# Performance work log

Measured on AMD Instinct MI355X. Metric: run time of the kernel, lower is better.

The kernel has to match this reference:

```python
import jax, jax.numpy as jnp
import numpy as np

B, M, S = 4, 1024, 1024
D, H, FF = 1024, 16, 4096
NE, P = 128, 1
HD = D // H
EPS = 1e-5


def _layer_norm(x, g, b):
    mu = x.mean(-1, keepdims=True)
    var = ((x - mu) ** 2).mean(-1, keepdims=True)
    return (x - mu) * jax.lax.rsqrt(var + EPS) * g + b


def _mha(q_in, kv_in, in_w, in_b, out_w, out_b):
    # torch nn.MultiheadAttention: packed in_proj_weight [3D, D], y = x @ W.T + b
    wq, wk, wv = in_w[:D], in_w[D:2 * D], in_w[2 * D:]
    bq, bk, bv = in_b[:D], in_b[D:2 * D], in_b[2 * D:]
    q = (q_in @ wq.T + bq).reshape(q_in.shape[0], q_in.shape[1], H, HD)
    k = (kv_in @ wk.T + bk).reshape(kv_in.shape[0], kv_in.shape[1], H, HD)
    v = (kv_in @ wv.T + bv).reshape(kv_in.shape[0], kv_in.shape[1], H, HD)
    scores = jnp.einsum('bqhd,bkhd->bhqk', q, k) / jnp.sqrt(jnp.float32(HD))
    attn = jax.nn.softmax(scores, axis=-1)
    o = jnp.einsum('bhqk,bkhd->bqhd', attn, v).reshape(q_in.shape[0], q_in.shape[1], D)
    return o @ out_w.T + out_b


def _soft_moe(h, phi, exp_w, exp_b):
    # h: [b, m, FF]; phi: [FF, n, p]
    logits = jnp.einsum('bmd,dnp->bmnp', h, phi)
    dispatch = jax.nn.softmax(logits, axis=1)  # over tokens m
    b, m, n, p = logits.shape
    combine = jax.nn.softmax(logits.reshape(b, m, n * p), axis=-1).reshape(b, m, n, p)
    slots = jnp.einsum('bmd,bmnp->bnpd', h, dispatch)  # [b, n, p, FF]
    y = jnp.einsum('bnpd,ndo->bnpo', slots, exp_w) + exp_b[None, :, None, :]  # [b, n, p, D]
    return jnp.einsum('bnpo,bmnp->bmo', y, combine)


def setup_inputs() -> dict:
    key = jax.random.key(0)
    ks = jax.random.split(key, 16)
    sc = 0.02

    def rn(k, shape):
        return jax.random.normal(k, shape, jnp.float32) * sc

    return {
        'tgt': jax.random.normal(ks[0], (B, M, D), jnp.float32),
        'memory': jax.random.normal(ks[1], (B, S, D), jnp.float32),
        'sa_in_w': rn(ks[2], (3 * D, D)), 'sa_in_b': jnp.zeros((3 * D,), jnp.float32),
        'sa_out_w': rn(ks[3], (D, D)), 'sa_out_b': jnp.zeros((D,), jnp.float32),
        'ca_in_w': rn(ks[4], (3 * D, D)), 'ca_in_b': jnp.zeros((3 * D,), jnp.float32),
        'ca_out_w': rn(ks[5], (D, D)), 'ca_out_b': jnp.zeros((D,), jnp.float32),
        'norm1_g': jnp.ones((D,), jnp.float32), 'norm1_b': jnp.zeros((D,), jnp.float32),
        'norm2_g': jnp.ones((D,), jnp.float32), 'norm2_b': jnp.zeros((D,), jnp.float32),
        'norm3_g': jnp.ones((D,), jnp.float32), 'norm3_b': jnp.zeros((D,), jnp.float32),
        'lin_w': rn(ks[6], (FF, D)), 'lin_b': jnp.zeros((FF,), jnp.float32),
        'phi': rn(ks[7], (FF, NE, P)),
        'exp_w': rn(ks[8], (NE, FF, D)), 'exp_b': jnp.zeros((NE, D), jnp.float32),
    }


def reference(tgt, memory, sa_in_w, sa_in_b, sa_out_w, sa_out_b,
              ca_in_w, ca_in_b, ca_out_w, ca_out_b,
              norm1_g, norm1_b, norm2_g, norm2_b, norm3_g, norm3_b,
              lin_w, lin_b, phi, exp_w, exp_b):
    # post-norm (norm_first=False), dropout=0 (eval)
    x = tgt
    x = _layer_norm(x + _mha(x, x, sa_in_w, sa_in_b, sa_out_w, sa_out_b), norm1_g, norm1_b)
    x = _layer_norm(x + _mha(x, memory, ca_in_w, ca_in_b, ca_out_w, ca_out_b), norm2_g, norm2_b)
    h = jax.nn.relu(x @ lin_w.T + lin_b)  # [B, M, FF]
    ff = _soft_moe(h, phi, exp_w, exp_b)  # [B, M, D]
    x = _layer_norm(x + ff, norm3_g, norm3_b)
    return x
```

## Files before the change

kernel.cpp:

```cpp
#include <hip/hip_runtime.h>
#include <cstdint>
#include <cstddef>

typedef unsigned short u16;
typedef unsigned int   u32;
typedef short bf16x8 __attribute__((ext_vector_type(8)));
typedef float f32x4  __attribute__((ext_vector_type(4)));
typedef u16   u16x8  __attribute__((ext_vector_type(8)));
typedef u16   u16x4  __attribute__((ext_vector_type(4)));
typedef u16   u16x2  __attribute__((ext_vector_type(2)));

constexpr int B_  = 4;
constexpr int M_  = 1024;
constexpr int S_  = 1024;
constexpr int D_  = 1024;
constexpr int H_  = 16;
constexpr int FF_ = 4096;
constexpr int NE_ = 128;

__device__ __forceinline__ u16 f2bf(float f) {
    u32 u = __builtin_bit_cast(u32, f);
    u = (u + 0x7fffu + ((u >> 16) & 1u)) >> 16;
    return (u16)u;
}
__device__ __forceinline__ float bf2f(u16 u) {
    u32 x = ((u32)u) << 16;
    return __builtin_bit_cast(float, x);
}
__device__ __forceinline__ void gload_lds16(const u16* g, u16* l) {
    __builtin_amdgcn_global_load_lds(
        (const __attribute__((address_space(1))) u32*)g,
        (__attribute__((address_space(3))) u32*)l, 16, 0, 0);
}

template<int OUT_BF16, int RELU, int HAS_BIAS>
__global__ __launch_bounds__(256) void gemm_bt_mfma(
    const u16* __restrict__ A, const u16* __restrict__ W,
    const float* __restrict__ bias, void* __restrict__ Cout,
    int K, int N, int lda, int ldw,
    size_t sA, size_t sW, size_t sC)
{
    __shared__ u16 As[128 * 32];
    __shared__ u16 Bs[128 * 32];
    const int tid = threadIdx.x;
    const int w = tid >> 6, l = tid & 63;
    const int bm = blockIdx.y * 128, bn = blockIdx.x * 128;
    const u16* Ab = A + (size_t)blockIdx.z * sA;
    const u16* Wb = W + (size_t)blockIdx.z * sW;

    const int wr = w >> 1, wc = w & 1;
    const int sr = l >> 2;
    const int sk = (l & 3) * 8;
    const u16* aG0 = Ab + (size_t)(bm + w * 16 + sr) * lda + sk;
    const u16* aG1 = Ab + (size_t)(bm + (w + 4) * 16 + sr) * lda + sk;
    const u16* bG0 = Wb + (size_t)(bn + w * 16 + sr) * ldw + sk;
    const u16* bG1 = Wb + (size_t)(bn + (w + 4) * 16 + sr) * ldw + sk;
    u16* aL0 = &As[w * 512];
    u16* aL1 = &As[(w + 4) * 512];
    u16* bL0 = &Bs[w * 512];
    u16* bL1 = &Bs[(w + 4) * 512];

    const int fr = l & 15;
    const int fk = (l >> 4) * 8;

    f32x4 acc[4][4];
#pragma unroll
    for (int i = 0; i < 4; ++i)
#pragma unroll
        for (int j = 0; j < 4; ++j)
#pragma unroll
            for (int q = 0; q < 4; ++q) acc[i][j][q] = 0.f;

    for (int k0 = 0; k0 < K; k0 += 32) {
        __syncthreads();
        gload_lds16(aG0, aL0);
        gload_lds16(aG1, aL1);
        gload_lds16(bG0, bL0);
        gload_lds16(bG1, bL1);
        aG0 += 32; aG1 += 32; bG0 += 32; bG1 += 32;
        __syncthreads();
        bf16x8 af[4], bfr[4];
#pragma unroll
        for (int m = 0; m < 4; ++m)
            af[m] = *(const bf16x8*)&As[(wr * 64 + m * 16 + fr) * 32 + fk];
#pragma unroll
        for (int n = 0; n < 4; ++n)
            bfr[n] = *(const bf16x8*)&Bs[(wc * 64 + n * 16 + fr) * 32 + fk];
#pragma unroll
        for (int m = 0; m < 4; ++m)
#pragma unroll
            for (int n = 0; n < 4; ++n)
                acc[m][n] = __builtin_amdgcn_mfma_f32_16x16x32_bf16(
                    af[m], bfr[n], acc[m][n], 0, 0, 0);
    }

    const int row0 = bm + wr * 64 + (l >> 4) * 4;
    const int col0 = bn + wc * 64;
#pragma unroll
    for (int n = 0; n < 4; ++n) {
        const int col = col0 + n * 16 + fr;
        float bv = 0.f;
        if (HAS_BIAS) bv = bias[col];
#pragma unroll
        for (int m = 0; m < 4; ++m) {
            const int row = row0 + m * 16;
#pragma unroll
            for (int j = 0; j < 4; ++j) {
                float v = acc[m][n][j] + bv;
                if (RELU) v = fmaxf(v, 0.f);
                const size_t idx = (size_t)blockIdx.z * sC + (size_t)(row + j) * N + col;
                if (OUT_BF16) ((u16*)Cout)[idx] = f2bf(v);
                else          ((float*)Cout)[idx] = v;
            }
        }
    }
}

__global__ __launch_bounds__(256) void flash_attn_kernel(
    const u16* __restrict__ Q, int qs,
    const u16* __restrict__ K, int ks,
    const u16* __restrict__ V, int vs,
    u16* __restrict__ O, int Slen)
{
    __shared__ u16 Qs[64][72];
    __shared__ u16 Ks[64][72];
    __shared__ u16 Vt[64][72];
    __shared__ u16 Pw[4][16][72];
    const int b = blockIdx.z, hh = blockIdx.y;
    const int m0 = blockIdx.x * 64;
    const int tid = threadIdx.x;
    const int w = tid >> 6, l = tid & 63;
    const int lq = l & 15, g = l >> 4;

    {
        const int row = tid >> 2, cg = (tid & 3) * 16;
        const u16* qp = Q + ((size_t)b * M_ + m0 + row) * qs + hh * 64 + cg;
        u16x8 v0 = *(const u16x8*)qp;
        u16x8 v1 = *(const u16x8*)(qp + 8);
        u16x8 o0, o1;
#pragma unroll
        for (int i = 0; i < 8; ++i) {
            o0[i] = f2bf(bf2f(v0[i]) * 0.125f);
            o1[i] = f2bf(bf2f(v1[i]) * 0.125f);
        }
        *(u16x8*)&Qs[row][cg]     = o0;
        *(u16x8*)&Qs[row][cg + 8] = o1;
    }
    __syncthreads();
    bf16x8 qf[2];
    qf[0] = *(const bf16x8*)&Qs[w * 16 + lq][g * 8];
    qf[1] = *(const bf16x8*)&Qs[w * 16 + lq][32 + g * 8];

    f32x4 acc_o[4];
#pragma unroll
    for (int nb = 0; nb < 4; ++nb)
#pragma unroll
        for (int j = 0; j < 4; ++j) acc_o[nb][j] = 0.f;
    float m_run = -1e30f, l_run = 0.f;

    const int kp = tid & 31, dg = tid >> 5;
    const int krow = tid >> 2, kcg = (tid & 3) * 16;

    for (int s0 = 0; s0 < Slen; s0 += 64) {
        __syncthreads();
        {
            const u16* kpp = K + ((size_t)b * Slen + s0 + krow) * ks + hh * 64 + kcg;
            *(u16x8*)&Ks[krow][kcg]     = *(const u16x8*)kpp;
            *(u16x8*)&Ks[krow][kcg + 8] = *(const u16x8*)(kpp + 8);
        }
        {
            const u16* vp0 = V + ((size_t)b * Slen + s0 + 2 * kp) * vs + hh * 64 + dg * 8;
            const u16* vp1 = vp0 + vs;
            u16x8 a = *(const u16x8*)vp0;
            u16x8 c = *(const u16x8*)vp1;
#pragma unroll
            for (int i = 0; i < 8; ++i) {
                u16x2 pk; pk[0] = a[i]; pk[1] = c[i];
                *(u16x2*)&Vt[dg * 8 + i][2 * kp] = pk;
            }
        }
        __syncthreads();

        f32x4 s4[4];
#pragma unroll
        for (int mb = 0; mb < 4; ++mb) {
            f32x4 z = {0.f, 0.f, 0.f, 0.f};
            bf16x8 a0 = *(const bf16x8*)&Ks[mb * 16 + lq][g * 8];
            bf16x8 a1 = *(const bf16x8*)&Ks[mb * 16 + lq][32 + g * 8];
            z = __builtin_amdgcn_mfma_f32_16x16x32_bf16(a0, qf[0], z, 0, 0, 0);
            z = __builtin_amdgcn_mfma_f32_16x16x32_bf16(a1, qf[1], z, 0, 0, 0);
            s4[mb] = z;
        }

        float pm = -1e30f;
#pragma unroll
        for (int mb = 0; mb < 4; ++mb)
#pragma unroll
            for (int j = 0; j < 4; ++j) pm = fmaxf(pm, s4[mb][j]);
        pm = fmaxf(pm, __shfl_xor(pm, 16));
        pm = fmaxf(pm, __shfl_xor(pm, 32));

        u16 pbf[4][4];
        float ls = 0.f;
        if (__all(pm - m_run <= 8.f)) {
#pragma unroll
            for (int mb = 0; mb < 4; ++mb)
#pragma unroll
                for (int j = 0; j < 4; ++j) {
                    float p = __expf(s4[mb][j] - m_run);
                    ls += p;
                    pbf[mb][j] = f2bf(p);
                }
            ls += __shfl_xor(ls, 16);
            ls += __shfl_xor(ls, 32);
            l_run += ls;
        } else {
            const float m_new = fmaxf(m_run, pm);
            const float alpha = __expf(m_run - m_new);
#pragma unroll
            for (int mb = 0; mb < 4; ++mb)
#pragma unroll
                for (int j = 0; j < 4; ++j) {
                    float p = __expf(s4[mb][j] - m_new);
                    ls += p;
                    pbf[mb][j] = f2bf(p);
                }
            ls += __shfl_xor(ls, 16);
            ls += __shfl_xor(ls, 32);
            l_run = l_run * alpha + ls;
            m_run = m_new;
            float al[4];
#pragma unroll
            for (int j = 0; j < 4; ++j) al[j] = __shfl(alpha, 4 * g + j);
#pragma unroll
            for (int nb = 0; nb < 4; ++nb)
#pragma unroll
                for (int j = 0; j < 4; ++j) acc_o[nb][j] *= al[j];
        }

#pragma unroll
        for (int mb = 0; mb < 4; ++mb) {
            u16x4 pk;
            pk[0] = pbf[mb][0]; pk[1] = pbf[mb][1];
            pk[2] = pbf[mb][2]; pk[3] = pbf[mb][3];
            *(u16x4*)&Pw[w][lq][mb * 16 + g * 4] = pk;
        }

#pragma unroll
        for (int kc = 0; kc < 2; ++kc) {
            bf16x8 pa = *(const bf16x8*)&Pw[w][lq][kc * 32 + g * 8];
#pragma unroll
            for (int nb = 0; nb < 4; ++nb) {
                bf16x8 bv = *(const bf16x8*)&Vt[nb * 16 + lq][kc * 32 + g * 8];
                acc_o[nb] = __builtin_amdgcn_mfma_f32_16x16x32_bf16(pa, bv, acc_o[nb], 0, 0, 0);
            }
        }
    }

    float linv[4];
#pragma unroll
    for (int j = 0; j < 4; ++j) linv[j] = 1.f / __shfl(l_run, 4 * g + j);
#pragma unroll
    for (int nb = 0; nb < 4; ++nb)
#pragma unroll
        for (int j = 0; j < 4; ++j) {
            const size_t row = (size_t)b * M_ + m0 + w * 16 + 4 * g + j;
            O[row * D_ + hh * 64 + nb * 16 + lq] = f2bf(acc_o[nb][j] * linv[j]);
        }
}

__global__ __launch_bounds__(256) void cvt_multi_kernel(
    const float* __restrict__ s0, u16* __restrict__ d0,
    const float* __restrict__ s1, u16* __restrict__ d1,
    const float* __restrict__ s2, u16* __restrict__ d2,
    const float* __restrict__ s3, u16* __restrict__ d3,
    const float* __restrict__ s4, u16* __restrict__ d4,
    const float* __restrict__ s5, u16* __restrict__ d5,
    const float* __restrict__ s6, u16* __restrict__ d6)
{
    int blk = blockIdx.x;
    const float* s; u16* d;
    if      (blk < 2048) { s = s0; d = d0; }
    else if (blk < 4096) { s = s1; d = d1; blk -= 2048; }
    else if (blk < 5632) { s = s2; d = d2; blk -= 4096; }
    else if (blk < 6144) { s = s3; d = d3; blk -= 5632; }
    else if (blk < 7680) { s = s4; d = d4; blk -= 6144; }
    else if (blk < 8192) { s = s5; d = d5; blk -= 7680; }
    else                 { s = s6; d = d6; blk -= 8192; }
    const size_t i = ((size_t)blk * 256 + threadIdx.x) * 8;
    float4 a = *(const float4*)(s + i);
    float4 b = *(const float4*)(s + i + 4);
    u16x8 o;
    o[0] = f2bf(a.x); o[1] = f2bf(a.y); o[2] = f2bf(a.z); o[3] = f2bf(a.w);
    o[4] = f2bf(b.x); o[5] = f2bf(b.y); o[6] = f2bf(b.z); o[7] = f2bf(b.w);
    *(u16x8*)(d + i) = o;
}

__global__ __launch_bounds__(256) void transpose_f32_bf16_kernel(
    const float* __restrict__ src, u16* __restrict__ dst, int R, int C,
    size_t sI, size_t sO)
{
    __shared__ u16 t[32][33];
    src += (size_t)blockIdx.z * sI;
    dst += (size_t)blockIdx.z * sO;
    const int c0 = blockIdx.x * 32, r0 = blockIdx.y * 32;
    const int x = threadIdx.x & 31, y = threadIdx.x >> 5;
    for (int i = y; i < 32; i += 8)
        t[i][x] = f2bf(src[(size_t)(r0 + i) * C + c0 + x]);
    __syncthreads();
    for (int i = y; i < 32; i += 8)
        dst[(size_t)(c0 + i) * R + r0 + x] = t[x][i];
}

__global__ __launch_bounds__(256) void transpose_bf16_kernel(
    const u16* __restrict__ src, u16* __restrict__ dst, int R, int C,
    size_t sI, size_t sO)
{
    __shared__ u16 t[32][33];
    src += (size_t)blockIdx.z * sI;
    dst += (size_t)blockIdx.z * sO;
    const int c0 = blockIdx.x * 32, r0 = blockIdx.y * 32;
    const int x = threadIdx.x & 31, y = threadIdx.x >> 5;
    for (int i = y; i < 32; i += 8)
        t[i][x] = src[(size_t)(r0 + i) * C + c0 + x];
    __syncthreads();
    for (int i = y; i < 32; i += 8)
        dst[(size_t)(c0 + i) * R + r0 + x] = t[x][i];
}

__global__ __launch_bounds__(256) void resid_ln_kernel(
    const float* __restrict__ X, const float* __restrict__ R,
    const float* __restrict__ g, const float* __restrict__ bt,
    float* __restrict__ Y, u16* __restrict__ Ybf)
{
    __shared__ float s1[4], s2[4];
    const size_t row = blockIdx.x;
    const int tid = threadIdx.x;
    const float4 x4 = *(const float4*)(X + row * 1024 + tid * 4);
    const float4 r4 = *(const float4*)(R + row * 1024 + tid * 4);
    float v[4] = {x4.x + r4.x, x4.y + r4.y, x4.z + r4.z, x4.w + r4.w};
    float s = v[0] + v[1] + v[2] + v[3];
    float q = v[0] * v[0] + v[1] * v[1] + v[2] * v[2] + v[3] * v[3];
#pragma unroll
    for (int off = 32; off; off >>= 1) {
        s += __shfl_xor(s, off);
        q += __shfl_xor(q, off);
    }
    if ((tid & 63) == 0) { s1[tid >> 6] = s; s2[tid >> 6] = q; }
    __syncthreads();
    s = s1[0] + s1[1] + s1[2] + s1[3];
    q = s2[0] + s2[1] + s2[2] + s2[3];
    const float mu = s * (1.f / 1024.f);
    const float var = q * (1.f / 1024.f) - mu * mu;
    const float rinv = rsqrtf(var + 1e-5f);
    const float4 g4 = *(const float4*)(g + tid * 4);
    const float4 b4 = *(const float4*)(bt + tid * 4);
    float o[4];
    o[0] = (v[0] - mu) * rinv * g4.x + b4.x;
    o[1] = (v[1] - mu) * rinv * g4.y + b4.y;
    o[2] = (v[2] - mu) * rinv * g4.z + b4.z;
    o[3] = (v[3] - mu) * rinv * g4.w + b4.w;
    *(float4*)(Y + row * 1024 + tid * 4) = *(float4*)o;
    if (Ybf) {
        u16x4 ob;
        ob[0] = f2bf(o[0]); ob[1] = f2bf(o[1]);
        ob[2] = f2bf(o[2]); ob[3] = f2bf(o[3]);
        *(u16x4*)(Ybf + row * 1024 + tid * 4) = ob;
    }
}

__global__ __launch_bounds__(256) void dispatch_softmax_T_kernel(
    const float* __restrict__ logitsP, u16* __restrict__ dispT)
{
    __shared__ float red[4];
    constexpr size_t CH = (size_t)B_ * M_ * NE_;
    const int n = blockIdx.x, b = blockIdx.y;
    u16* O = dispT + ((size_t)b * NE_ + n) * M_;
    const int tid = threadIdx.x;
    float v[4];
#pragma unroll
    for (int i = 0; i < 4; ++i) {
        const size_t idx = (size_t)(b * M_ + tid + 256 * i) * NE_ + n;
        v[i] = logitsP[idx] + logitsP[CH + idx] + logitsP[2 * CH + idx] + logitsP[3 * CH + idx];
    }
    float mx = fmaxf(fmaxf(v[0], v[1]), fmaxf(v[2], v[3]));
#pragma unroll
    for (int off = 32; off; off >>= 1) mx = fmaxf(mx, __shfl_xor(mx, off));
    if ((tid & 63) == 0) red[tid >> 6] = mx;
    __syncthreads();
    mx = fmaxf(fmaxf(red[0], red[1]), fmaxf(red[2], red[3]));
    __syncthreads();
    float e[4], s = 0.f;
#pragma unroll
    for (int i = 0; i < 4; ++i) { e[i] = __expf(v[i] - mx); s += e[i]; }
#pragma unroll
    for (int off = 32; off; off >>= 1) s += __shfl_xor(s, off);
    if ((tid & 63) == 0) red[tid >> 6] = s;
    __syncthreads();
    s = red[0] + red[1] + red[2] + red[3];
    const float inv = 1.f / s;
#pragma unroll
    for (int i = 0; i < 4; ++i) O[tid + 256 * i] = f2bf(e[i] * inv);
}

__global__ __launch_bounds__(64) void combine_softmax_kernel(
    const float* __restrict__ logitsP, u16* __restrict__ comb)
{
    constexpr size_t CH = (size_t)B_ * M_ * NE_;
    const size_t row = blockIdx.x;
    const int lane = threadIdx.x;
    const size_t i0 = row * NE_ + lane;
    const size_t i1 = i0 + 64;
    float a = logitsP[i0] + logitsP[CH + i0] + logitsP[2 * CH + i0] + logitsP[3 * CH + i0];
    float c = logitsP[i1] + logitsP[CH + i1] + logitsP[2 * CH + i1] + logitsP[3 * CH + i1];
    float mx = fmaxf(a, c);
#pragma unroll
    for (int off = 32; off; off >>= 1) mx = fmaxf(mx, __shfl_xor(mx, off));
    float e0 = __expf(a - mx), e1 = __expf(c - mx);
    float s = e0 + e1;
#pragma unroll
    for (int off = 32; off; off >>= 1) s += __shfl_xor(s, off);
    const float inv = 1.f / s;
    comb[row * NE_ + lane]      = f2bf(e0 * inv);
    comb[row * NE_ + lane + 64] = f2bf(e1 * inv);
}

__global__ __launch_bounds__(256) void expert_partial_kernel(
    const float* __restrict__ slots, const float* __restrict__ exp_w,
    float* __restrict__ part)
{
    __shared__ float sl[4][512];
    const int n = blockIdx.x;
    const int c = blockIdx.y;
    const int f0 = c * 512;
    const int t = threadIdx.x;
    for (int i = t; i < 2048; i += 256) {
        const int b = i >> 9, f = i & 511;
        sl[b][f] = slots[((size_t)b * NE_ + n) * FF_ + f0 + f];
    }
    __syncthreads();
    const int d4 = t * 4;
    const float* wp = exp_w + ((size_t)n * FF_ + f0) * D_ + d4;
    f32x4 acc[4];
#pragma unroll
    for (int b = 0; b < 4; ++b)
#pragma unroll
        for (int j = 0; j < 4; ++j) acc[b][j] = 0.f;
#pragma unroll 4
    for (int f = 0; f < 512; ++f) {
        const float4 w4 = *(const float4*)wp;
        wp += D_;
#pragma unroll
        for (int b = 0; b < 4; ++b) {
            const float s = sl[b][f];
            acc[b][0] = fmaf(s, w4.x, acc[b][0]);
            acc[b][1] = fmaf(s, w4.y, acc[b][1]);
            acc[b][2] = fmaf(s, w4.z, acc[b][2]);
            acc[b][3] = fmaf(s, w4.w, acc[b][3]);
        }
    }
#pragma unroll
    for (int b = 0; b < 4; ++b)
        *(f32x4*)&part[(((size_t)c * 4 + b) * NE_ + n) * D_ + d4] = acc[b];
}

__global__ __launch_bounds__(256) void reduce_yT_kernel(
    const float* __restrict__ part, const float* __restrict__ exp_b,
    u16* __restrict__ yT)
{
    __shared__ float tile[32][33];
    const int d0 = blockIdx.x * 32, n0 = blockIdx.y * 32, b = blockIdx.z;
    const int x = threadIdx.x & 31, y = threadIdx.x >> 5;
    for (int i = y; i < 32; i += 8) {
        const int n = n0 + i;
        float s = exp_b[(size_t)n * D_ + d0 + x];
#pragma unroll
        for (int c = 0; c < 8; ++c)
            s += part[(((size_t)c * 4 + b) * NE_ + n) * D_ + d0 + x];
        tile[i][x] = s;
    }
    __syncthreads();
    for (int i = y; i < 32; i += 8)
        yT[((size_t)b * D_ + d0 + i) * NE_ + n0 + x] = f2bf(tile[x][i]);
}

extern "C" void kernel_launch(void* const* d_in, const int* in_sizes, int n_in,
                              void* d_out, int out_size, void* d_ws, size_t ws_size,
                              hipStream_t stream)
{
    const float* tgt      = (const float*)d_in[0];
    const float* memry    = (const float*)d_in[1];
    const float* sa_in_w  = (const float*)d_in[2];
    const float* sa_in_b  = (const float*)d_in[3];
    const float* sa_out_w = (const float*)d_in[4];
    const float* sa_out_b = (const float*)d_in[5];
    const float* ca_in_w  = (const float*)d_in[6];
    const float* ca_in_b  = (const float*)d_in[7];
    const float* ca_out_w = (const float*)d_in[8];
    const float* ca_out_b = (const float*)d_in[9];
    const float* norm1_g  = (const float*)d_in[10];
    const float* norm1_b  = (const float*)d_in[11];
    const float* norm2_g  = (const float*)d_in[12];
    const float* norm2_b  = (const float*)d_in[13];
    const float* norm3_g  = (const float*)d_in[14];
    const float* norm3_b  = (const float*)d_in[15];
    const float* lin_w    = (const float*)d_in[16];
    const float* lin_b    = (const float*)d_in[17];
    const float* phi      = (const float*)d_in[18];
    const float* exp_w    = (const float*)d_in[19];
    const float* exp_b    = (const float*)d_in[20];

    float* ws = (float*)d_ws;
    u16*   qkv_bf  = (u16*)(ws);
    float* proj    = ws + 6291456;
    float* x1      = ws + 10485760;
    float* x2      = ws + 14680064;
    float* logitsP = ws + 18874368;
    float* part    = ws + 20971520;
    u16*   h_bf    = (u16*)(ws + 25165824);
    u16*   hT_bf   = (u16*)(ws + 33554432);
    u16*   obuf_bf = (u16*)(ws + 41943040);
    u16*   x1_bf   = (u16*)(ws + 44040192);
    u16*   x2_bf   = (u16*)(ws + 46137344);
    u16*   tgt_bf  = (u16*)(ws + 48234496);
    u16*   mem_bf  = (u16*)(ws + 50331648);
    u16*   dispT   = (u16*)(ws + 52428800);
    u16*   comb_bf = (u16*)(ws + 52690944);
    u16*   yT_bf   = (u16*)(ws + 52953088);
    u16*   slots_n = 0; float* slots = ws + 53215232;
    (void)slots_n;
    u16*   w_sa_in = (u16*)(ws + 55312384);
    u16*   w_sa_out= (u16*)(ws + 56885248);
    u16*   w_ca_in = (u16*)(ws + 57409536);
    u16*   w_ca_out= (u16*)(ws + 58982400);
    u16*   w_lin   = (u16*)(ws + 59506688);
    u16*   phiT    = (u16*)(ws + 61603840);

    cvt_multi_kernel<<<10240, 256, 0, stream>>>(
        tgt, tgt_bf, memry, mem_bf, sa_in_w, w_sa_in, sa_out_w, w_sa_out,
        ca_in_w, w_ca_in, ca_out_w, w_ca_out, lin_w, w_lin);
    transpose_f32_bf16_kernel<<<dim3(4, 128, 1), 256, 0, stream>>>(phi, phiT, 4096, 128, 0, 0);

    gemm_bt_mfma<1, 0, 1><<<dim3(24, 32, 1), 256, 0, stream>>>(
        tgt_bf, w_sa_in, sa_in_b, qkv_bf, 1024, 3072, 1024, 1024, 0, 0, 0);
    flash_attn_kernel<<<dim3(16, 16, 4), 256, 0, stream>>>(
        qkv_bf, 3072, qkv_bf + 1024, 3072, qkv_bf + 2048, 3072, obuf_bf, S_);
    gemm_bt_mfma<0, 0, 1><<<dim3(8, 32, 1), 256, 0, stream>>>(
        obuf_bf, w_sa_out, sa_out_b, proj, 1024, 1024, 1024, 1024, 0, 0, 0);
    resid_ln_kernel<<<4096, 256, 0, stream>>>(tgt, proj, norm1_g, norm1_b, x1, x1_bf);

    u16* qca_bf = qkv_bf;
    u16* kvca_bf = qkv_bf + (size_t)4096 * 1024;
    gemm_bt_mfma<1, 0, 1><<<dim3(8, 32, 1), 256, 0, stream>>>(
        x1_bf, w_ca_in, ca_in_b, qca_bf, 1024, 1024, 1024, 1024, 0, 0, 0);
    gemm_bt_mfma<1, 0, 1><<<dim3(16, 32, 1), 256, 0, stream>>>(
        mem_bf, w_ca_in + (size_t)1024 * 1024, ca_in_b + 1024,
        kvca_bf, 1024, 2048, 1024, 1024, 0, 0, 0);
    flash_attn_kernel<<<dim3(16, 16, 4), 256, 0, stream>>>(
        qca_bf, 1024, kvca_bf, 2048, kvca_bf + 1024, 2048, obuf_bf, S_);
    gemm_bt_mfma<0, 0, 1><<<dim3(8, 32, 1), 256, 0, stream>>>(
        obuf_bf, w_ca_out, ca_out_b, proj, 1024, 1024, 1024, 1024, 0, 0, 0);
    resid_ln_kernel<<<4096, 256, 0, stream>>>(x1, proj, norm2_g, norm2_b, x2, x2_bf);

    gemm_bt_mfma<1, 1, 1><<<dim3(32, 32, 1), 256, 0, stream>>>(
        x2_bf, w_lin, lin_b, h_bf, 1024, 4096, 1024, 1024, 0, 0, 0);
    gemm_bt_mfma<0, 0, 0><<<dim3(1, 32, 4), 256, 0, stream>>>(
        h_bf, phiT, nullptr, logitsP, 1024, 128, 4096, 4096,
        1024, 1024, (size_t)B_ * M_ * NE_);
    dispatch_softmax_T_kernel<<<dim3(NE_, B_), 256, 0, stream>>>(logitsP, dispT);
    combine_softmax_kernel<<<dim3(B_ * M_), 64, 0, stream>>>(logitsP, comb_bf);
    transpose_bf16_kernel<<<dim3(128, 32, 4), 256, 0, stream>>>(
        h_bf, hT_bf, 1024, 4096, (size_t)M_ * FF_, (size_t)M_ * FF_);
    gemm_bt_mfma<0, 0, 0><<<dim3(32, 1, 4), 256, 0, stream>>>(
        dispT, hT_bf, nullptr, slots, 1024, 4096, 1024, 1024,
        (size_t)NE_ * M_, (size_t)FF_ * M_, (size_t)NE_ * FF_);
    expert_partial_kernel<<<dim3(NE_, 8), 256, 0, stream>>>(slots, exp_w, part);
    reduce_yT_kernel<<<dim3(32, 4, 4), 256, 0, stream>>>(part, exp_b, yT_bf);
    gemm_bt_mfma<0, 0, 0><<<dim3(8, 8, 4), 256, 0, stream>>>(
        comb_bf, yT_bf, nullptr, proj, 128, 1024, 128, 128,
        (size_t)M_ * NE_, (size_t)D_ * NE_, (size_t)M_ * D_);
    resid_ln_kernel<<<4096, 256, 0, stream>>>(x2, proj, norm3_g, norm3_b,
                                              (float*)d_out, nullptr);
}
```

Measured before the change: 839.0 us.

## Add 256x256 tiled MFMA GEMM with triple-buffered LDS for large projections

Introduces a 512-thread GEMM kernel with 256x256 output tiles, a three-stage LDS ring fed by direct global-to-LDS loads, swizzled LDS layout, and barrier/setprio-interleaved MFMA phases. It replaces the 128x128 GEMM for the self-attention QKV projection, the cross-attention KV projection and the FFN linear+ReLU. The larger tiles raise data reuse per loaded byte and the ring overlaps loads with compute. The cost is fewer blocks (192, 128 and 256) on a many-CU GPU, so parts of the device may sit idle. Higher register use from 128 accumulators per thread also limits occupancy to one block.

```diff
diff --git a/kernel.cpp b/kernel.cpp
--- a/kernel.cpp
+++ b/kernel.cpp
@@ -31,6 +31,128 @@
     __builtin_amdgcn_global_load_lds(
         (const __attribute__((address_space(1))) u32*)g,
         (__attribute__((address_space(3))) u32*)l, 16, 0, 0);
+}
+
+template<int RELU>
+__global__ __launch_bounds__(512, 1) void gemm256_mfma(
+    const u16* __restrict__ A, const u16* __restrict__ W,
+    const float* __restrict__ bias, u16* __restrict__ C,
+    int K, int N, int lda, int ldw)
+{
+    __shared__ u16 lds[49152];
+    const int tid = threadIdx.x;
+    const int w = tid >> 6, l = tid & 63;
+    const int wr = w >> 2, wc = w & 3;
+    const int fr = l & 15, g = l >> 4;
+    const int bm = blockIdx.y * 256, bn = blockIdx.x * 256;
+
+    const int qcol = (((l & 3) ^ ((l >> 3) & 3))) * 8;
+    const int srow = w * 16 + (l >> 2);
+    const u16* aG0 = A + (size_t)(bm + srow) * lda + qcol;
+    const u16* aG1 = aG0 + (size_t)128 * lda;
+    const u16* bG0 = W + (size_t)(bn + srow) * ldw + qcol;
+    const u16* bG1 = bG0 + (size_t)128 * ldw;
+    const int wofs = w * 512;
+
+    const int qsw = (g ^ ((fr >> 1) & 3)) * 8;
+    const int aoff = (wr * 128 + fr) * 32 + qsw;
+    const int boff = (wc * 64 + fr) * 32 + qsw;
+
+    f32x4 acc[8][4];
+#pragma unroll
+    for (int i = 0; i < 8; ++i)
+#pragma unroll
+        for (int j = 0; j < 4; ++j)
+#pragma unroll
+            for (int q = 0; q < 4; ++q) acc[i][j][q] = 0.f;
+
+    gload_lds16(aG0, &lds[0 + wofs]);
+    gload_lds16(aG1, &lds[4096 + wofs]);
+    gload_lds16(bG0, &lds[24576 + wofs]);
+    gload_lds16(bG1, &lds[24576 + 4096 + wofs]);
+    aG0 += 32; aG1 += 32; bG0 += 32; bG1 += 32;
+    gload_lds16(aG0, &lds[8192 + wofs]);
+    gload_lds16(aG1, &lds[8192 + 4096 + wofs]);
+    gload_lds16(bG0, &lds[32768 + wofs]);
+    gload_lds16(bG1, &lds[32768 + 4096 + wofs]);
+    aG0 += 32; aG1 += 32; bG0 += 32; bG1 += 32;
+    asm volatile("s_waitcnt vmcnt(4)" ::: "memory");
+    __builtin_amdgcn_s_barrier();
+    __builtin_amdgcn_sched_barrier(0);
+
+    int rb = 0;
+
+#define G256_STEP(ISSUE_, VMOPT_)                                            \
+  {                                                                          \
+    const int wb_ = (rb >= 1) ? rb - 1 : 2;                                  \
+    const u16* Ab_ = &lds[rb * 8192];                                        \
+    const u16* Bb_ = &lds[24576 + rb * 8192];                                \
+    u16* Aw_ = &lds[wb_ * 8192];                                             \
+    u16* Bw_ = &lds[24576 + wb_ * 8192];                                     \
+    bf16x8 af_[4], bf_[4];                                                   \
+    _Pragma("unroll") for (int mf = 0; mf < 4; ++mf)                         \
+      af_[mf] = *(const bf16x8*)(Ab_ + aoff + mf * 512);                     \
+    _Pragma("unroll") for (int nf = 0; nf < 4; ++nf)                         \
+      bf_[nf] = *(const bf16x8*)(Bb_ + boff + nf * 512);                     \
+    if (ISSUE_) {                                                            \
+      gload_lds16(aG0, Aw_ + wofs);                                          \
+      gload_lds16(aG1, Aw_ + 4096 + wofs);                                   \
+    }                                                                        \
+    __builtin_amdgcn_s_barrier();                                            \
+    __builtin_amdgcn_sched_barrier(0);                                       \
+    __builtin_amdgcn_s_setprio(1);                                           \
+    _Pragma("unroll") for (int mf = 0; mf < 4; ++mf)                         \
+      _Pragma("unroll") for (int nf = 0; nf < 4; ++nf)                       \
+        acc[mf][nf] = __builtin_amdgcn_mfma_f32_16x16x32_bf16(               \
+            af_[mf], bf_[nf], acc[mf][nf], 0, 0, 0);                         \
+    __builtin_amdgcn_s_setprio(0);                                           \
+    __builtin_amdgcn_s_barrier();                                            \
+    __builtin_amdgcn_sched_barrier(0);                                       \
+    _Pragma("unroll") for (int mf = 0; mf < 4; ++mf)                         \
+      af_[mf] = *(const bf16x8*)(Ab_ + aoff + 2048 + mf * 512);              \
+    if (ISSUE_) {                                                            \
+      gload_lds16(bG0, Bw_ + wofs);                                          \
+      gload_lds16(bG1, Bw_ + 4096 + wofs);                                   \
+      aG0 += 32; aG1 += 32; bG0 += 32; bG1 += 32;                            \
+    }                                                                        \
+    VMOPT_                                                                   \
+    __builtin_amdgcn_s_barrier();                                            \
+    __builtin_amdgcn_sched_barrier(0);                                       \
+    __builtin_amdgcn_s_setprio(1);                                           \
+    _Pragma("unroll") for (int mf = 0; mf < 4; ++mf)                         \
+      _Pragma("unroll") for (int nf = 0; nf < 4; ++nf)                       \
+        acc[mf + 4][nf] = __builtin_amdgcn_mfma_f32_16x16x32_bf16(           \
+            af_[mf], bf_[nf], acc[mf + 4][nf], 0, 0, 0);                     \
+    __builtin_amdgcn_s_setprio(0);                                           \
+    __builtin_amdgcn_s_barrier();                                            \
+    __builtin_amdgcn_sched_barrier(0);                                       \
+    rb = (rb == 2) ? 0 : rb + 1;                                             \
+  }
+
+    const int nstep = K >> 5;
+    for (int t = 0; t < nstep - 2; ++t) {
+        G256_STEP(1, asm volatile("s_waitcnt vmcnt(4)" ::: "memory");)
+    }
+    G256_STEP(0, asm volatile("s_waitcnt vmcnt(0)" ::: "memory");)
+    G256_STEP(0, )
+#undef G256_STEP
+
+    const int row0 = bm + wr * 128 + g * 4;
+    const int col0 = bn + wc * 64 + fr;
+#pragma unroll
+    for (int nf = 0; nf < 4; ++nf) {
+        const int col = col0 + nf * 16;
+        const float bv = bias[col];
+#pragma unroll
+        for (int mf = 0; mf < 8; ++mf) {
+#pragma unroll
+            for (int j = 0; j < 4; ++j) {
+                float v = acc[mf][nf][j] + bv;
+                if (RELU) v = fmaxf(v, 0.f);
+                C[(size_t)(row0 + mf * 16 + j) * N + col] = f2bf(v);
+            }
+        }
+    }
 }
 
 template<int OUT_BF16, int RELU, int HAS_BIAS>
@@ -527,8 +649,7 @@
     u16*   dispT   = (u16*)(ws + 52428800);
     u16*   comb_bf = (u16*)(ws + 52690944);
     u16*   yT_bf   = (u16*)(ws + 52953088);
-    u16*   slots_n = 0; float* slots = ws + 53215232;
-    (void)slots_n;
+    float* slots   = ws + 53215232;
     u16*   w_sa_in = (u16*)(ws + 55312384);
     u16*   w_sa_out= (u16*)(ws + 56885248);
     u16*   w_ca_in = (u16*)(ws + 57409536);
@@ -541,8 +662,8 @@
         ca_in_w, w_ca_in, ca_out_w, w_ca_out, lin_w, w_lin);
     transpose_f32_bf16_kernel<<<dim3(4, 128, 1), 256, 0, stream>>>(phi, phiT, 4096, 128, 0, 0);
 
-    gemm_bt_mfma<1, 0, 1><<<dim3(24, 32, 1), 256, 0, stream>>>(
-        tgt_bf, w_sa_in, sa_in_b, qkv_bf, 1024, 3072, 1024, 1024, 0, 0, 0);
+    gemm256_mfma<0><<<dim3(12, 16, 1), 512, 0, stream>>>(
+        tgt_bf, w_sa_in, sa_in_b, qkv_bf, 1024, 3072, 1024, 1024);
     flash_attn_kernel<<<dim3(16, 16, 4), 256, 0, stream>>>(
         qkv_bf, 3072, qkv_bf + 1024, 3072, qkv_bf + 2048, 3072, obuf_bf, S_);
     gemm_bt_mfma<0, 0, 1><<<dim3(8, 32, 1), 256, 0, stream>>>(
@@ -553,17 +674,17 @@
     u16* kvca_bf = qkv_bf + (size_t)4096 * 1024;
     gemm_bt_mfma<1, 0, 1><<<dim3(8, 32, 1), 256, 0, stream>>>(
         x1_bf, w_ca_in, ca_in_b, qca_bf, 1024, 1024, 1024, 1024, 0, 0, 0);
-    gemm_bt_mfma<1, 0, 1><<<dim3(16, 32, 1), 256, 0, stream>>>(
+    gemm256_mfma<0><<<dim3(8, 16, 1), 512, 0, stream>>>(
         mem_bf, w_ca_in + (size_t)1024 * 1024, ca_in_b + 1024,
-        kvca_bf, 1024, 2048, 1024, 1024, 0, 0, 0);
+        kvca_bf, 1024, 2048, 1024, 1024);
     flash_attn_kernel<<<dim3(16, 16, 4), 256, 0, stream>>>(
         qca_bf, 1024, kvca_bf, 2048, kvca_bf + 1024, 2048, obuf_bf, S_);
     gemm_bt_mfma<0, 0, 1><<<dim3(8, 32, 1), 256, 0, stream>>>(
         obuf_bf, w_ca_out, ca_out_b, proj, 1024, 1024, 1024, 1024, 0, 0, 0);
     resid_ln_kernel<<<4096, 256, 0, stream>>>(x1, proj, norm2_g, norm2_b, x2, x2_bf);
 
-    gemm_bt_mfma<1, 1, 1><<<dim3(32, 32, 1), 256, 0, stream>>>(
-        x2_bf, w_lin, lin_b, h_bf, 1024, 4096, 1024, 1024, 0, 0, 0);
+    gemm256_mfma<1><<<dim3(16, 16, 1), 512, 0, stream>>>(
+        x2_bf, w_lin, lin_b, h_bf, 1024, 4096, 1024, 1024);
     gemm_bt_mfma<0, 0, 0><<<dim3(1, 32, 4), 256, 0, stream>>>(
         h_bf, phiT, nullptr, logitsP, 1024, 128, 4096, 4096,
         1024, 1024, (size_t)B_ * M_ * NE_);
```

New measurement: 832.0 us. No clear change (-0.8%).
